# Optimization experiments

Hardware: AMD Instinct MI355X
Metric: run time of the kernel (lower is better)

Reference implementation:

```python
import jax, jax.numpy as jnp
import numpy as np

B, N, M, C, H = 2, 256, 512, 256, 8
Dh = C // H          # head dim = 32
F = 256              # frequency_embedding_size
MAX_PERIOD = 10000.0


def setup_inputs() -> dict:
    rng = jax.random.key(0)
    ks = jax.random.split(rng, 12)
    s = 0.02

    def w(k, shape):
        return jax.random.normal(k, shape, jnp.float32) * s

    inp = {
        "query": jax.random.normal(ks[0], (B, N, C), jnp.float32),
        "key": jax.random.normal(ks[1], (B, M, C), jnp.float32),
        "query_pos": jax.random.uniform(ks[2], (B, N, M), jnp.float32),
        # attention projections (torch Linear stores W as (out,in))
        "Wq": w(ks[3], (C, C)), "bq": jnp.zeros((C,), jnp.float32),
        "Wk": w(ks[4], (C, C)),
        "Wv": w(ks[5], (C, C)), "bv": jnp.zeros((C,), jnp.float32),
        "Wo": w(ks[6], (C, C)), "bo": jnp.zeros((C,), jnp.float32),
        # ScalarEmbedder MLP: Linear(F, C) -> SiLU -> Linear(C, C)
        "W1": w(ks[7], (C, F)), "b1": jnp.zeros((C,), jnp.float32),
        "W2": w(ks[8], (C, C)), "b2": jnp.zeros((C,), jnp.float32),
        "freqs": jnp.exp(-np.log(MAX_PERIOD) * jnp.arange(F // 2, dtype=jnp.float32) / (F // 2)),
    }
    return inp


def reference(query, key, query_pos, Wq, bq, Wk, Wv, bv, Wo, bo, W1, b1, W2, b2, freqs):
    scale = Dh ** (-0.5)
    # projections -> (B, H, N/M, Dh)
    q = (query @ Wq.T + bq).reshape(B, N, H, Dh).transpose(0, 2, 1, 3)
    k = (key @ Wk.T).reshape(B, M, H, Dh).transpose(0, 2, 1, 3)
    v = (key @ Wv.T + bv).reshape(B, M, H, Dh).transpose(0, 2, 1, 3)
    # scalar positional embedding per (n, m) pair
    t = query_pos.reshape(-1)                              # (B*N*M,)
    tf = t[:, None] * freqs                                # (B*N*M, F/2)
    emb = jnp.concatenate([jnp.cos(tf), jnp.sin(tf)], -1)  # (B*N*M, F)
    pe = jax.nn.silu(emb @ W1.T + b1) @ W2.T + b2          # (B*N*M, C)
    pe = pe.reshape(B, N, M, H, Dh).transpose(0, 3, 1, 2, 4)  # (B,H,N,M,Dh)
    # gated scores: (q[:,:,:,None] * pe) . k  ==  einsum over d
    attn = jnp.einsum('bhnd,bhnmd,bhmd->bhnm', q, pe, k) * scale
    attn = jax.nn.softmax(attn, axis=-1)
    x = jnp.einsum('bhnm,bhmd->bhnd', attn, v)             # (B,H,N,Dh)
    x = x.transpose(0, 2, 1, 3).reshape(B, N, C)
    return x @ Wo.T + bo + query
```

## Files before the change

### kernel.cpp

```cpp
#include <hip/hip_runtime.h>

#define Bn 2
#define Nn 256
#define Mn 512
#define Cn 256
#define Hn 8
#define MT 64
#define SCALE_ 0.17677669529663687f
#define INV2PI 0.15915494309189535f

typedef short bf16x8 __attribute__((ext_vector_type(8)));
typedef short bf16x4 __attribute__((ext_vector_type(4)));
typedef float f32x4 __attribute__((ext_vector_type(4)));

static __device__ __forceinline__ float b2f(short s) {
    unsigned u = ((unsigned)(unsigned short)s) << 16;
    return __builtin_bit_cast(float, u);
}
static __device__ __forceinline__ short f2b(float f) {
    unsigned u = __builtin_bit_cast(unsigned, f);
    u += 0x7fffu + ((u >> 16) & 1u);
    return (short)(u >> 16);
}
static __device__ __forceinline__ void async16(const void* g, void* l) {
    __builtin_amdgcn_global_load_lds(
        (const __attribute__((address_space(1))) unsigned int*)g,
        (__attribute__((address_space(3))) unsigned int*)l, 16, 0, 0);
}

__global__ __launch_bounds__(256) void prep2(
        const float* __restrict__ key, const float* __restrict__ Wk,
        const float* __restrict__ Wv, const float* __restrict__ bv,
        const float* __restrict__ W1, const float* __restrict__ W2,
        short* __restrict__ W1b, short* __restrict__ W2b,
        short* __restrict__ kpb, short* __restrict__ vpb) {
    __shared__ float arow[32][Cn];
    const int bid = blockIdx.x;
    const int t = threadIdx.x;
    if (bid < 64) {
        const int half = bid >> 5;
        const int off = (bid & 31) * 2048 + t * 8;
        const float* src = half ? W2 : W1;
        short* dst = half ? W2b : W1b;
        const float4 a = *(const float4*)(src + off);
        const float4 c = *(const float4*)(src + off + 4);
        bf16x8 p;
        p[0] = f2b(a.x); p[1] = f2b(a.y); p[2] = f2b(a.z); p[3] = f2b(a.w);
        p[4] = f2b(c.x); p[5] = f2b(c.y); p[6] = f2b(c.z); p[7] = f2b(c.w);
        *(bf16x8*)(dst + off) = p;
        return;
    }
    const int isv = bid >= 320;
    const int id = bid - (isv ? 320 : 64);
    const int r0 = (id >> 3) * 32, c0 = (id & 7) * 32;
    const float* W = isv ? Wv : Wk;
    #pragma unroll
    for (int i = 0; i < 32; ++i) arow[i][t] = key[(size_t)(r0 + i) * Cn + t];
    __syncthreads();
    const int col = c0 + (t & 31);
    const int rs = t >> 5;
    float a4[4] = {0.f, 0.f, 0.f, 0.f};
    const float* wr = W + (size_t)col * Cn;
    for (int k = 0; k < Cn; k += 4) {
        const float4 wv = *(const float4*)(wr + k);
        #pragma unroll
        for (int i = 0; i < 4; ++i) {
            const int r = rs * 4 + i;
            a4[i] += arow[r][k] * wv.x + arow[r][k+1] * wv.y
                   + arow[r][k+2] * wv.z + arow[r][k+3] * wv.w;
        }
    }
    if (!isv) {
        const int bk = r0 >> 9, mm0 = (r0 & 511) + rs * 4;
        char* base = (char*)kpb + (size_t)bk * Mn * Cn * 2;
        #pragma unroll
        for (int i = 0; i < 4; ++i) {
            const int m = mm0 + i;
            *(short*)(base + m * 512 + ((col * 2) ^ ((m & 7) << 4))) = f2b(a4[i]);
        }
    } else {
        const float bvv = bv[col];
        #pragma unroll
        for (int i = 0; i < 4; ++i)
            vpb[(size_t)(r0 + rs * 4 + i) * Cn + col] = f2b(a4[i] + bvv);
    }
}

__global__ __launch_bounds__(512, 1) void fused_attn(
        const float* __restrict__ query, const float* __restrict__ Wq,
        const float* __restrict__ bq, const short* __restrict__ kpb,
        const short* __restrict__ vpb, const float* __restrict__ qpos,
        const short* __restrict__ W1b, const short* __restrict__ W2b,
        const float* __restrict__ b1, const float* __restrict__ b2,
        const float* __restrict__ freqs, const float* __restrict__ Wo,
        const float* __restrict__ bo, float* __restrict__ xout) {
    __shared__ __align__(16) char embS[2][MT * 512];
    __shared__ __align__(16) char kS[MT * 512];
    __shared__ float tposS[Mn];
    __shared__ float fbuf[128];
    __shared__ float qbuf[Cn];
    __shared__ float b2buf[Cn];
    __shared__ float scb2[Hn * MT];
    __shared__ float pacc[512];
    __shared__ float corrS[Hn], lS[Hn];

    const int t = threadIdx.x;
    const int lane = t & 63;
    const int w = t >> 6;
    const int lr = lane & 15, lg = lane >> 4;

    const int qrow = ((blockIdx.x & 7) << 6) | (blockIdx.x >> 3);
    const int b = qrow >> 8;

    const int cA = w * 32 + lr, cB = cA + 16;
    const short* w1p0 = W1b + (size_t)cA * Cn + lg * 8;
    const short* w1p1 = W1b + (size_t)cB * Cn + lg * 8;
    const short* w2p0 = W2b + (size_t)cA * Cn + lg * 8;
    const short* w2p1 = W2b + (size_t)cB * Cn + lg * 8;
    const float b1v0 = b1[cA], b1v1 = b1[cB];

    auto emb_compute = [&](int m0w, char* buf) {
        const int m = t >> 3, fg = t & 7;
        const float tv = tposS[(m0w + m) & (Mn - 1)];
        char* rowp = buf + m * 512;
        const int sw = (m & 7) << 4;
        #pragma unroll
        for (int j8 = 0; j8 < 2; ++j8) {
            bf16x8 pc, ps;
            #pragma unroll
            for (int e = 0; e < 8; ++e) {
                const float xr = tv * fbuf[fg * 16 + j8 * 8 + e];
                pc[e] = f2b(__builtin_amdgcn_cosf(xr));
                ps[e] = f2b(__builtin_amdgcn_sinf(xr));
            }
            *(bf16x8*)(rowp + ((fg * 32 + j8 * 16) ^ sw)) = pc;
            *(bf16x8*)(rowp + ((256 + fg * 32 + j8 * 16) ^ sw)) = ps;
        }
    };
    auto stage_k = [&](int m0w) {
        const size_t tbase = ((size_t)(b * Mn + (m0w & (Mn - 1)))) * Cn * 2;
        #pragma unroll
        for (int i = 0; i < 4; ++i) {
            const int seg = (i * 8 + w) * 1024;
            async16((const char*)kpb + tbase + seg + lane * 16, kS + seg);
        }
    };

    tposS[t] = qpos[(size_t)qrow * Mn + t];
    if (t < 128) fbuf[t] = freqs[t] * INV2PI;
    if (t < 256) {
        b2buf[t] = b2[t];
        scb2[t] = query[(size_t)qrow * Cn + t];
    }
    __syncthreads();
    {
        const int c = t & 255, half = t >> 8;
        const float* wr = Wq + (size_t)c * Cn + half * 128;
        const float* xb = scb2 + half * 128;
        float s = 0.f;
        for (int k = 0; k < 128; k += 4) {
            const float4 wv = *(const float4*)(wr + k);
            s += xb[k] * wv.x + xb[k+1] * wv.y + xb[k+2] * wv.z + xb[k+3] * wv.w;
        }
        pacc[t] = s;
    }
    __syncthreads();
    if (t < 256) qbuf[t] = (pacc[t] + pacc[t + 256] + bq[t]) * SCALE_;
    emb_compute(0, embS[0]);
    stage_k(0);

    float m_run = -1e30f, l_run = 0.f;
    float xacc = 0.f;
    bf16x8 wreg[16];

    for (int tix = 0; tix < Mn / MT; ++tix) {
        const int m0 = tix * MT;
        char* bufc = embS[tix & 1];
        char* bufn = embS[(tix + 1) & 1];

        __syncthreads();
        if (tix > 0 && t < 256) xacc = xacc * corrS[t >> 5] + pacc[t] + pacc[t + 256];

        {
            int woff = 0;
            asm volatile("" : "+v"(woff));
            #pragma unroll
            for (int kk = 0; kk < 8; ++kk) {
                wreg[kk] = *(const bf16x8*)(w1p0 + woff + kk * 32);
                wreg[8 + kk] = *(const bf16x8*)(w1p1 + woff + kk * 32);
            }
        }
        f32x4 acc[4][2];
        #pragma unroll
        for (int pb = 0; pb < 4; ++pb) {
            acc[pb][0] = (f32x4){0.f, 0.f, 0.f, 0.f};
            acc[pb][1] = (f32x4){0.f, 0.f, 0.f, 0.f};
        }
        #pragma unroll
        for (int pb = 0; pb < 4; ++pb) {
            const int row = pb * 16 + lr;
            const int sw = (row & 7) << 4;
            const char* rowp = bufc + row * 512;
            #pragma unroll
            for (int kk = 0; kk < 8; ++kk) {
                const bf16x8 a = *(const bf16x8*)(rowp + ((lg * 16 + kk * 64) ^ sw));
                acc[pb][0] = __builtin_amdgcn_mfma_f32_16x16x32_bf16(a, wreg[kk],     acc[pb][0], 0, 0, 0);
                acc[pb][1] = __builtin_amdgcn_mfma_f32_16x16x32_bf16(a, wreg[8 + kk], acc[pb][1], 0, 0, 0);
            }
        }
        emb_compute(m0 + MT, bufn);
        __syncthreads();

        {
            int woff = 0;
            asm volatile("" : "+v"(woff));
            #pragma unroll
            for (int kk = 0; kk < 8; ++kk) {
                wreg[kk] = *(const bf16x8*)(w2p0 + woff + kk * 32);
                wreg[8 + kk] = *(const bf16x8*)(w2p1 + woff + kk * 32);
            }
        }
        #pragma unroll
        for (int pb = 0; pb < 4; ++pb) {
            #pragma unroll
            for (int jb = 0; jb < 2; ++jb) {
                const float bv = jb ? b1v1 : b1v0;
                const int j = w * 32 + jb * 16 + lr;
                #pragma unroll
                for (int r = 0; r < 4; ++r) {
                    const int row = pb * 16 + lg * 4 + r;
                    float hv = acc[pb][jb][r] + bv;
                    hv = hv / (1.f + __expf(-hv));
                    *(short*)(bufc + row * 512 + ((j * 2) ^ ((row & 7) << 4))) = f2b(hv);
                }
            }
        }
        __syncthreads();

        {
            float b2a[8];
            #pragma unroll
            for (int i = 0; i < 8; ++i)
                b2a[i] = b2buf[w * 32 + (i >> 2) * 16 + lg * 4 + (i & 3)];
            #pragma unroll
            for (int mb = 0; mb < 4; ++mb)
                #pragma unroll
                for (int cb = 0; cb < 2; ++cb)
                    #pragma unroll
                    for (int r = 0; r < 4; ++r)
                        acc[mb][cb][r] = b2a[cb * 4 + r];
        }
        #pragma unroll
        for (int mb = 0; mb < 4; ++mb) {
            const int row = mb * 16 + lr;
            const int sw = (row & 7) << 4;
            const char* rowp = bufc + row * 512;
            #pragma unroll
            for (int kk = 0; kk < 8; ++kk) {
                const bf16x8 a = *(const bf16x8*)(rowp + ((lg * 16 + kk * 64) ^ sw));
                acc[mb][0] = __builtin_amdgcn_mfma_f32_16x16x32_bf16(wreg[kk],     a, acc[mb][0], 0, 0, 0);
                acc[mb][1] = __builtin_amdgcn_mfma_f32_16x16x32_bf16(wreg[8 + kk], a, acc[mb][1], 0, 0, 0);
            }
        }

        {
            float qa[8];
            #pragma unroll
            for (int i = 0; i < 8; ++i)
                qa[i] = qbuf[w * 32 + (i >> 2) * 16 + lg * 4 + (i & 3)];
            #pragma unroll
            for (int mb = 0; mb < 4; ++mb) {
                const int m = mb * 16 + lr;
                const int sw = (m & 7) << 4;
                const char* kr = kS + m * 512;
                const int cc0 = (w * 32 + lg * 4) * 2;
                const bf16x4 k0 = *(const bf16x4*)(kr + (cc0 ^ sw));
                const bf16x4 k1 = *(const bf16x4*)(kr + ((cc0 + 32) ^ sw));
                float partial = 0.f;
                #pragma unroll
                for (int r = 0; r < 4; ++r) {
                    partial += qa[r] * b2f(k0[r]) * acc[mb][0][r]
                             + qa[4 + r] * b2f(k1[r]) * acc[mb][1][r];
                }
                partial += __shfl_xor(partial, 16);
                partial += __shfl_xor(partial, 32);
                if (lg == 0) scb2[w * MT + m] = partial;
            }
        }

        {
            const float s = scb2[w * MT + lane];
            float tmax = s;
            #pragma unroll
            for (int msk = 1; msk < 64; msk <<= 1) tmax = fmaxf(tmax, __shfl_xor(tmax, msk));
            const float mnew = fmaxf(m_run, tmax);
            const float corr = __expf(m_run - mnew);
            const float e = __expf(s - mnew);
            scb2[w * MT + lane] = e;
            float ss = e;
            #pragma unroll
            for (int msk = 1; msk < 64; msk <<= 1) ss += __shfl_xor(ss, msk);
            l_run = l_run * corr + ss;
            m_run = mnew;
            if (lane == 0) corrS[w] = corr;
        }
        __syncthreads();

        stage_k(m0 + MT);

        {
            const int c = t & 255, half = t >> 8;
            const int h = c >> 5;
            const short* vrow = vpb + ((size_t)(b * Mn + m0 + half * 32)) * Cn + c;
            const float* wr2 = scb2 + h * MT + half * 32;
            float s = 0.f;
            #pragma unroll
            for (int i = 0; i < 8; ++i) {
                const float4 wa = *(const float4*)(wr2 + i * 4);
                s += wa.x * b2f(vrow[(size_t)(i * 4 + 0) * Cn])
                   + wa.y * b2f(vrow[(size_t)(i * 4 + 1) * Cn])
                   + wa.z * b2f(vrow[(size_t)(i * 4 + 2) * Cn])
                   + wa.w * b2f(vrow[(size_t)(i * 4 + 3) * Cn]);
            }
            pacc[t] = s;
        }
    }
    __syncthreads();
    if (t < 256) xacc = xacc * corrS[t >> 5] + pacc[t] + pacc[t + 256];

    if (lane == 0) lS[w] = l_run;
    __syncthreads();
    if (t < 256) scb2[t] = xacc / lS[t >> 5];
    __syncthreads();
    {
        const int j = t & 255, half = t >> 8;
        const float* wr = Wo + (size_t)j * Cn + half * 128;
        const float* xb = scb2 + half * 128;
        float s = 0.f;
        for (int k = 0; k < 128; k += 4) {
            const float4 wv = *(const float4*)(wr + k);
            s += xb[k] * wv.x + xb[k+1] * wv.y + xb[k+2] * wv.z + xb[k+3] * wv.w;
        }
        pacc[t] = s;
    }
    __syncthreads();
    if (t < 256)
        xout[(size_t)qrow * Cn + t] = pacc[t] + pacc[t + 256] + bo[t]
                                    + query[(size_t)qrow * Cn + t];
}

extern "C" void kernel_launch(void* const* d_in, const int* in_sizes, int n_in,
                              void* d_out, int out_size, void* d_ws, size_t ws_size,
                              hipStream_t stream) {
    const float* query = (const float*)d_in[0];
    const float* key   = (const float*)d_in[1];
    const float* qpos  = (const float*)d_in[2];
    const float* Wq    = (const float*)d_in[3];
    const float* bq    = (const float*)d_in[4];
    const float* Wk    = (const float*)d_in[5];
    const float* Wv    = (const float*)d_in[6];
    const float* bv    = (const float*)d_in[7];
    const float* Wo    = (const float*)d_in[8];
    const float* bo    = (const float*)d_in[9];
    const float* W1    = (const float*)d_in[10];
    const float* b1    = (const float*)d_in[11];
    const float* W2    = (const float*)d_in[12];
    const float* b2    = (const float*)d_in[13];
    const float* freqs = (const float*)d_in[14];
    float* out = (float*)d_out;

    char* ws = (char*)d_ws;
    short* kpb = (short*)(ws);
    short* vpb = (short*)(ws + 524288);
    short* W1b = (short*)(ws + 1048576);
    short* W2b = (short*)(ws + 1179648);

    prep2<<<576, 256, 0, stream>>>(key, Wk, Wv, bv, W1, W2, W1b, W2b, kpb, vpb);
    fused_attn<<<Bn * Nn, 512, 0, stream>>>(query, Wq, bq, kpb, vpb, qpos,
                                            W1b, W2b, b1, b2, freqs, Wo, bo, out);
}
```

Measured before the change: 333.7 us.

## Single-buffer embedding tile and relax launch bounds to allow two blocks per CU

Drops the double-buffered embedding LDS tile for a single buffer, computed at the start of each iteration instead of being prefetched during the first MLP GEMM. With LDS roughly halved and the min-blocks constraint removed from launch bounds, more than one 512-thread block could fit per CU, so other blocks hide latency in place of intra-block overlap. It also moves the W1 register reload to right after the second GEMM so it is prefetched for the next tile, issues the first K staging earlier, and replaces the SiLU division with a hardware reciprocal. The risk is losing the trig/MFMA overlap and extra register pressure if the compiler now targets higher occupancy.

```diff
diff --git a/kernel.cpp b/kernel.cpp
--- a/kernel.cpp
+++ b/kernel.cpp
@@ -86,7 +86,7 @@
     }
 }
 
-__global__ __launch_bounds__(512, 1) void fused_attn(
+__global__ __launch_bounds__(512) void fused_attn(
         const float* __restrict__ query, const float* __restrict__ Wq,
         const float* __restrict__ bq, const short* __restrict__ kpb,
         const short* __restrict__ vpb, const float* __restrict__ qpos,
@@ -94,7 +94,7 @@
         const float* __restrict__ b1, const float* __restrict__ b2,
         const float* __restrict__ freqs, const float* __restrict__ Wo,
         const float* __restrict__ bo, float* __restrict__ xout) {
-    __shared__ __align__(16) char embS[2][MT * 512];
+    __shared__ __align__(16) char embS[MT * 512];
     __shared__ __align__(16) char kS[MT * 512];
     __shared__ float tposS[Mn];
     __shared__ float fbuf[128];
@@ -119,24 +119,6 @@
     const short* w2p1 = W2b + (size_t)cB * Cn + lg * 8;
     const float b1v0 = b1[cA], b1v1 = b1[cB];
 
-    auto emb_compute = [&](int m0w, char* buf) {
-        const int m = t >> 3, fg = t & 7;
-        const float tv = tposS[(m0w + m) & (Mn - 1)];
-        char* rowp = buf + m * 512;
-        const int sw = (m & 7) << 4;
-        #pragma unroll
-        for (int j8 = 0; j8 < 2; ++j8) {
-            bf16x8 pc, ps;
-            #pragma unroll
-            for (int e = 0; e < 8; ++e) {
-                const float xr = tv * fbuf[fg * 16 + j8 * 8 + e];
-                pc[e] = f2b(__builtin_amdgcn_cosf(xr));
-                ps[e] = f2b(__builtin_amdgcn_sinf(xr));
-            }
-            *(bf16x8*)(rowp + ((fg * 32 + j8 * 16) ^ sw)) = pc;
-            *(bf16x8*)(rowp + ((256 + fg * 32 + j8 * 16) ^ sw)) = ps;
-        }
-    };
     auto stage_k = [&](int m0w) {
         const size_t tbase = ((size_t)(b * Mn + (m0w & (Mn - 1)))) * Cn * 2;
         #pragma unroll
@@ -152,6 +134,7 @@
         b2buf[t] = b2[t];
         scb2[t] = query[(size_t)qrow * Cn + t];
     }
+    stage_k(0);
     __syncthreads();
     {
         const int c = t & 255, half = t >> 8;
@@ -166,30 +149,40 @@
     }
     __syncthreads();
     if (t < 256) qbuf[t] = (pacc[t] + pacc[t + 256] + bq[t]) * SCALE_;
-    emb_compute(0, embS[0]);
-    stage_k(0);
 
     float m_run = -1e30f, l_run = 0.f;
     float xacc = 0.f;
     bf16x8 wreg[16];
+    #pragma unroll
+    for (int kk = 0; kk < 8; ++kk) {
+        wreg[kk] = *(const bf16x8*)(w1p0 + kk * 32);
+        wreg[8 + kk] = *(const bf16x8*)(w1p1 + kk * 32);
+    }
 
     for (int tix = 0; tix < Mn / MT; ++tix) {
         const int m0 = tix * MT;
-        char* bufc = embS[tix & 1];
-        char* bufn = embS[(tix + 1) & 1];
-
+
+        {
+            const int m = t >> 3, fg = t & 7;
+            const float tv = tposS[m0 + m];
+            char* rowp = embS + m * 512;
+            const int sw = (m & 7) << 4;
+            #pragma unroll
+            for (int j8 = 0; j8 < 2; ++j8) {
+                bf16x8 pc, ps;
+                #pragma unroll
+                for (int e = 0; e < 8; ++e) {
+                    const float xr = tv * fbuf[fg * 16 + j8 * 8 + e];
+                    pc[e] = f2b(__builtin_amdgcn_cosf(xr));
+                    ps[e] = f2b(__builtin_amdgcn_sinf(xr));
+                }
+                *(bf16x8*)(rowp + ((fg * 32 + j8 * 16) ^ sw)) = pc;
+                *(bf16x8*)(rowp + ((256 + fg * 32 + j8 * 16) ^ sw)) = ps;
+            }
+        }
         __syncthreads();
         if (tix > 0 && t < 256) xacc = xacc * corrS[t >> 5] + pacc[t] + pacc[t + 256];
 
-        {
-            int woff = 0;
-            asm volatile("" : "+v"(woff));
-            #pragma unroll
-            for (int kk = 0; kk < 8; ++kk) {
-                wreg[kk] = *(const bf16x8*)(w1p0 + woff + kk * 32);
-                wreg[8 + kk] = *(const bf16x8*)(w1p1 + woff + kk * 32);
-            }
-        }
         f32x4 acc[4][2];
         #pragma unroll
         for (int pb = 0; pb < 4; ++pb) {
@@ -200,7 +193,7 @@
         for (int pb = 0; pb < 4; ++pb) {
             const int row = pb * 16 + lr;
             const int sw = (row & 7) << 4;
-            const char* rowp = bufc + row * 512;
+            const char* rowp = embS + row * 512;
             #pragma unroll
             for (int kk = 0; kk < 8; ++kk) {
                 const bf16x8 a = *(const bf16x8*)(rowp + ((lg * 16 + kk * 64) ^ sw));
@@ -208,7 +201,6 @@
                 acc[pb][1] = __builtin_amdgcn_mfma_f32_16x16x32_bf16(a, wreg[8 + kk], acc[pb][1], 0, 0, 0);
             }
         }
-        emb_compute(m0 + MT, bufn);
         __syncthreads();
 
         {
@@ -229,9 +221,9 @@
                 #pragma unroll
                 for (int r = 0; r < 4; ++r) {
                     const int row = pb * 16 + lg * 4 + r;
-                    float hv = acc[pb][jb][r] + bv;
-                    hv = hv / (1.f + __expf(-hv));
-                    *(short*)(bufc + row * 512 + ((j * 2) ^ ((row & 7) << 4))) = f2b(hv);
+                    const float hv = acc[pb][jb][r] + bv;
+                    const float sg = __builtin_amdgcn_rcpf(1.f + __expf(-hv));
+                    *(short*)(embS + row * 512 + ((j * 2) ^ ((row & 7) << 4))) = f2b(hv * sg);
                 }
             }
         }
@@ -254,12 +246,21 @@
         for (int mb = 0; mb < 4; ++mb) {
             const int row = mb * 16 + lr;
             const int sw = (row & 7) << 4;
-            const char* rowp = bufc + row * 512;
+            const char* rowp = embS + row * 512;
             #pragma unroll
             for (int kk = 0; kk < 8; ++kk) {
                 const bf16x8 a = *(const bf16x8*)(rowp + ((lg * 16 + kk * 64) ^ sw));
                 acc[mb][0] = __builtin_amdgcn_mfma_f32_16x16x32_bf16(wreg[kk],     a, acc[mb][0], 0, 0, 0);
                 acc[mb][1] = __builtin_amdgcn_mfma_f32_16x16x32_bf16(wreg[8 + kk], a, acc[mb][1], 0, 0, 0);
+            }
+        }
+        {
+            int woff = 0;
+            asm volatile("" : "+v"(woff));
+            #pragma unroll
+            for (int kk = 0; kk < 8; ++kk) {
+                wreg[kk] = *(const bf16x8*)(w1p0 + woff + kk * 32);
+                wreg[8 + kk] = *(const bf16x8*)(w1p1 + woff + kk * 32);
             }
         }
 
```

Result: faster. 318.4 us (-4.6%).
